# Performance work log

Measured on AMD Instinct MI355X. Metric: run time of the kernel, lower is better.

## Reference

```python
import jax, jax.numpy as jnp
import numpy as np

H = 256      # hidden_dim
D = 64       # dim_dynamic
ND = 2       # num_dynamic
PR = 7       # pooler_resolution
S = PR * PR  # 49 spatial positions
B = 4800     # N * nr_boxes
P = H * D    # num_params
EPS = 1e-5


def setup_inputs() -> dict:
    key = jax.random.key(0)
    ks = jax.random.split(key, 32)
    def w(k, shape):
        return jax.random.normal(k, shape, dtype=jnp.float32) * 0.02
    inp = {
        "pro_features": jax.random.normal(ks[0], (1, B, H), jnp.float32),
        "roi_features": jax.random.normal(ks[1], (S, B, H), jnp.float32),
        "pos_xywh": jax.random.normal(ks[2], (1, B, H), jnp.float32),
        "pos_img": jax.random.normal(ks[3], (S, B, H), jnp.float32),
        "pos_local": jax.random.uniform(ks[4], (PR, PR), jnp.float32),
        "bboxes_xywh": jax.random.uniform(ks[5], (B, 4), jnp.float32, minval=0.2, maxval=1.0),
        # dynamic_layer: H -> ND*P
        "Wd": w(ks[6], (H, ND * P)), "bd": jnp.zeros((ND * P,), jnp.float32),
        # query_scale MLP (2 layers, H->H->H)
        "Wqs1": w(ks[7], (H, H)), "bqs1": jnp.zeros((H,), jnp.float32),
        "Wqs2": w(ks[8], (H, H)), "bqs2": jnp.zeros((H,), jnp.float32),
        # ref_point_head MLP (2 layers, H->H->2)
        "Wr1": w(ks[9], (H, H)), "br1": jnp.zeros((H,), jnp.float32),
        "Wr2": w(ks[10], (H, 2)), "br2": jnp.zeros((2,), jnp.float32),
        # ca_qpos_proj / ca_kpos_proj
        "Wq": w(ks[11], (H, H)), "bq": jnp.zeros((H,), jnp.float32),
        "Wk": w(ks[12], (H, H)), "bk": jnp.zeros((H,), jnp.float32),
        # layer norms
        "g1": jnp.ones((D,), jnp.float32), "be1": jnp.zeros((D,), jnp.float32),
        "g2": jnp.ones((H,), jnp.float32), "be2": jnp.zeros((H,), jnp.float32),
        "g3": jnp.ones((H,), jnp.float32), "be3": jnp.zeros((H,), jnp.float32),
        # out_layer: (H*S) -> H
        "Wo": w(ks[13], (H * S, H)), "bo": jnp.zeros((H,), jnp.float32),
    }
    return inp


def _ln(x, g, b):
    m = jnp.mean(x, axis=-1, keepdims=True)
    v = jnp.mean((x - m) ** 2, axis=-1, keepdims=True)
    return (x - m) * jax.lax.rsqrt(v + EPS) * g + b


def reference(pro_features, roi_features, pos_xywh, pos_img, pos_local, bboxes_xywh,
              Wd, bd, Wqs1, bqs1, Wqs2, bqs2, Wr1, br1, Wr2, br2,
              Wq, bq, Wk, bk, g1, be1, g2, be2, g3, be3, Wo, bo):
    # (S,B,H) -> (B,S,H)
    features_pos = jnp.transpose(pos_img @ Wq + bq, (1, 0, 2))
    features = jnp.transpose(roi_features, (1, 0, 2))
    # dynamic parameters: (1,B,ND*P) -> (B,1,ND*P)
    parameters = jnp.transpose(pro_features @ Wd + bd, (1, 0, 2))
    # query_scale MLP
    pos_t = jax.nn.relu(pro_features @ Wqs1 + bqs1) @ Wqs2 + bqs2  # (1,B,H)
    px = pos_xywh[..., :H] * pos_t                                 # (1,B,H)
    # ref_point_head -> sigmoid
    ref = jax.nn.sigmoid(jax.nn.relu(pro_features @ Wr1 + br1) @ Wr2 + br2)  # (1,B,2)
    bb = bboxes_xywh.reshape(1, -1, 4)
    hi = px[..., H // 2:] * (ref[..., 0] / bb[..., 2])[..., None]
    lo = px[..., :H // 2] * (ref[..., 1] / bb[..., 3])[..., None]
    px = jnp.concatenate([lo, hi], axis=-1)
    # (B,1,H) * (1,S,1) -> (B,S,H)
    px = jnp.transpose(px, (1, 0, 2)) * pos_local.reshape(-1)[None, :, None]
    param1_pos = px @ Wk + bk                                      # (B,S,H)
    param1 = parameters[:, :, :P].reshape(-1, H, D)                # (B,H,D)
    param2 = parameters[:, :, P:].reshape(-1, D, H)                # (B,D,H)
    f = jnp.einsum('bsh,bhd->bsd', features, param1)               # (B,S,D)
    fp = jnp.sum(features_pos * param1_pos, axis=-1)               # (B,S)
    f = f + fp[:, :, None]
    f = jax.nn.relu(_ln(f, g1, be1))
    f = jnp.einsum('bsd,bdh->bsh', f, param2)                      # (B,S,H)
    f = jax.nn.relu(_ln(f, g2, be2))
    f = f.reshape(f.shape[0], -1) @ Wo + bo                        # (B,H)
    f = jax.nn.relu(_ln(f, g3, be3))
    return f
```

## Files before the change

kernel.cpp:

```cpp
#include <hip/hip_runtime.h>
#include <hip/hip_bf16.h>

#define HH 256
#define DD 64
#define SS 49
#define BB 4800
#define PP 16384
#define NDP 32768
#define KWO 12544
#define MPAD 4864
#define SK 8
#define KCH 1568

typedef unsigned int u32;
typedef unsigned short u16;
typedef __attribute__((ext_vector_type(8))) short bf16x8;
typedef __attribute__((ext_vector_type(4))) float f32x4;

__device__ __forceinline__ float bf2f(__hip_bfloat16 h) { return __bfloat162float(h); }

__device__ __forceinline__ void load_lds16(const void* g, void* l) {
  __builtin_amdgcn_global_load_lds(
      (const __attribute__((address_space(1))) unsigned int*)g,
      (__attribute__((address_space(3))) unsigned int*)l, 16, 0, 0);
}

__device__ __forceinline__ int nperm(int n) {
  if (n < PP) { int h = n >> 6, d = n & 63; return d * HH + h; }
  int r = n - PP; int d = r >> 8, h = r & 255; return PP + h * DD + d;
}

__device__ __forceinline__ float wave_sum64(float v) {
#pragma unroll
  for (int off = 32; off > 0; off >>= 1) v += __shfl_xor(v, off);
  return v;
}

__device__ __forceinline__ float block_sum256(float v, float* red) {
  v = wave_sum64(v);
  int w = threadIdx.x >> 6;
  if ((threadIdx.x & 63) == 0) red[w] = v;
  __syncthreads();
  float r = red[0] + red[1] + red[2] + red[3];
  __syncthreads();
  return r;
}

__global__ void k0_prep(const float* __restrict__ Wq, const float* __restrict__ bk,
                        const float* __restrict__ bq, float* __restrict__ w2c2) {
  __shared__ float red[4];
  int k = blockIdx.x, h = threadIdx.x;
  float v = Wq[k * HH + h];
  float s = block_sum256(v * bk[h], red);
  if (h == 0) w2c2[k] = s;
  if (k == 0) {
    float s2 = block_sum256(bq[h] * bk[h], red);
    if (h == 0) w2c2[HH] = s2;
  }
}

__global__ __launch_bounds__(256) void kc_w1(
    const float* __restrict__ Wqs1, const float* __restrict__ Wqs2,
    const float* __restrict__ Wr1, const float* __restrict__ Wk,
    const float* __restrict__ Wq,
    u16* __restrict__ w1t, u16* __restrict__ w2t, u16* __restrict__ wr1t,
    u16* __restrict__ wkt, u16* __restrict__ wqh) {
  int t = threadIdx.x;
  int zi = blockIdx.z;
  if (zi == 4) {
    int row = blockIdx.y * 32 + (t >> 3), col = blockIdx.x * 32 + (t & 7) * 4;
    float4 v = *(const float4*)&Wq[row * HH + col];
    union { u16 u[4]; uint2 q; } pk;
    __hip_bfloat16 hb;
    hb = __float2bfloat16(v.x); pk.u[0] = *(u16*)&hb;
    hb = __float2bfloat16(v.y); pk.u[1] = *(u16*)&hb;
    hb = __float2bfloat16(v.z); pk.u[2] = *(u16*)&hb;
    hb = __float2bfloat16(v.w); pk.u[3] = *(u16*)&hb;
    *(uint2*)&wqh[row * HH + col] = pk.q;
    return;
  }
  const float* src = (zi == 0) ? Wqs1 : (zi == 1) ? Wqs2 : (zi == 2) ? Wr1 : Wk;
  u16* dst = (zi == 0) ? w1t : (zi == 1) ? w2t : (zi == 2) ? wr1t : wkt;
  __shared__ float tile[32][33];
  int n0 = blockIdx.x * 32, k0 = blockIdx.y * 32;
  {
    int kk = t >> 3, nn = (t & 7) * 4;
    float4 v = *(const float4*)&src[(k0 + kk) * HH + n0 + nn];
    tile[kk][nn + 0] = v.x;
    tile[kk][nn + 1] = v.y;
    tile[kk][nn + 2] = v.z;
    tile[kk][nn + 3] = v.w;
  }
  __syncthreads();
  {
    int nn = t >> 3, kk = (t & 7) * 4;
    union { u16 u[4]; uint2 q; } pk;
#pragma unroll
    for (int i = 0; i < 4; ++i) {
      __hip_bfloat16 hb = __float2bfloat16(tile[kk + i][nn]);
      pk.u[i] = *(u16*)&hb;
    }
    *(uint2*)&dst[(n0 + nn) * HH + k0 + kk] = pk.q;
  }
}

__device__ __forceinline__ void g_gemm(const u16* aLb, const u16* __restrict__ Bg,
                                       int wm, int wn, int lg, int lr,
                                       f32x4 acc[2][4]) {
#pragma unroll
  for (int k0 = 0; k0 < HH; k0 += 32) {
    int colb = (k0 + (lg << 3)) << 1;
    bf16x8 af[2];
#pragma unroll
    for (int mi = 0; mi < 2; ++mi) {
      int row = wm * 32 + mi * 16 + lr;
      af[mi] = *(const bf16x8*)((const char*)aLb + (row << 9) +
                                (colb ^ ((row & 7) << 4)));
    }
    bf16x8 bfr[4];
#pragma unroll
    for (int ni = 0; ni < 4; ++ni) {
      int n = wn * 64 + ni * 16 + lr;
      bfr[ni] = *(const bf16x8*)&Bg[n * HH + k0 + (lg << 3)];
    }
#pragma unroll
    for (int mi = 0; mi < 2; ++mi)
#pragma unroll
      for (int ni = 0; ni < 4; ++ni)
        acc[mi][ni] = __builtin_amdgcn_mfma_f32_16x16x32_bf16(af[mi], bfr[ni], acc[mi][ni], 0, 0, 0);
  }
}

__device__ __forceinline__ void c_write(u16* xLb, f32x4 acc[2][4],
                                        const float* __restrict__ bias, bool dorelu,
                                        int wm, int wn, int lg, int lr) {
#pragma unroll
  for (int ni = 0; ni < 4; ++ni) {
    int col = wn * 64 + ni * 16 + lr;
    float bv = bias ? bias[col] : 0.f;
#pragma unroll
    for (int mi = 0; mi < 2; ++mi) {
#pragma unroll
      for (int j = 0; j < 4; ++j) {
        int row = wm * 32 + mi * 16 + (lg << 2) + j;
        float v = acc[mi][ni][j] + bv;
        if (dorelu) v = fmaxf(v, 0.f);
        __hip_bfloat16 hb = __float2bfloat16(v);
        *(u16*)((char*)xLb + (row << 9) + (((col << 1)) ^ ((row & 7) << 4))) = *(u16*)&hb;
      }
    }
  }
}

__global__ __launch_bounds__(512) void k1_mfma(
    const u16* __restrict__ proh, const float* __restrict__ posx,
    const float* __restrict__ bbox,
    const u16* __restrict__ w1t, const u16* __restrict__ w2t,
    const u16* __restrict__ wr1t, const u16* __restrict__ wkt,
    const u16* __restrict__ wqh,
    const float* __restrict__ bqs1, const float* __restrict__ bqs2,
    const float* __restrict__ br1, const float* __restrict__ Wr2,
    const float* __restrict__ br2, const float* __restrict__ bq,
    float* __restrict__ z, float* __restrict__ c1) {
  __shared__ u16 aL[16384];
  __shared__ u16 xL[16384];
  __shared__ float red0[512], red1[512];
  __shared__ float scLoL[64], scHiL[64];
  const int t = threadIdx.x;
  const int w = t >> 6, l = t & 63;
  const int lg = l >> 4, lr = l & 15;
  const int wm = w >> 2, wn = w & 3;
  const int m0 = blockIdx.x * 64;

#pragma unroll
  for (int i = 0; i < 4; ++i) {
    int c = i * 512 + t;
    int a = c * 16;
    int row = a >> 9, x0 = a & 511;
    int src = (m0 + row) * HH + ((x0 ^ ((row & 7) << 4)) >> 1);
    load_lds16(proh + src, (char*)aL + (size_t)(i * 512 + (w << 6)) * 16);
  }
  __syncthreads();

  {
    f32x4 acc[2][4] = {};
    g_gemm(aL, wr1t, wm, wn, lg, lr, acc);
    c_write(xL, acc, br1, true, wm, wn, lg, lr);
  }
  __syncthreads();
  {
    int row = t & 63, seg = t >> 6;
    float s0 = 0.f, s1 = 0.f;
#pragma unroll 8
    for (int hh = 0; hh < 32; ++hh) {
      int h = seg * 32 + hh;
      float rv = bf2f(*(const __hip_bfloat16*)((const char*)xL + (row << 9) +
                                               (((h << 1)) ^ ((row & 7) << 4))));
      s0 = fmaf(rv, Wr2[h * 2 + 0], s0);
      s1 = fmaf(rv, Wr2[h * 2 + 1], s1);
    }
    red0[row * 8 + seg] = s0;
    red1[row * 8 + seg] = s1;
  }
  __syncthreads();
  if (t < 64) {
    float s0 = br2[0], s1 = br2[1];
#pragma unroll
    for (int k = 0; k < 8; ++k) {
      s0 += red0[t * 8 + k];
      s1 += red1[t * 8 + k];
    }
    float r0 = 1.f / (1.f + __expf(-s0));
    float r1 = 1.f / (1.f + __expf(-s1));
    scHiL[t] = r0 / bbox[(m0 + t) * 4 + 2];
    scLoL[t] = r1 / bbox[(m0 + t) * 4 + 3];
  }
  f32x4 acc1[2][4] = {};
  g_gemm(aL, w1t, wm, wn, lg, lr, acc1);
  __syncthreads();
  c_write(xL, acc1, bqs1, true, wm, wn, lg, lr);
  __syncthreads();
  f32x4 accp[2][4] = {};
  g_gemm(xL, w2t, wm, wn, lg, lr, accp);
  __syncthreads();
#pragma unroll
  for (int ni = 0; ni < 4; ++ni) {
    int col = wn * 64 + ni * 16 + lr;
    float bv = bqs2[col];
#pragma unroll
    for (int mi = 0; mi < 2; ++mi) {
#pragma unroll
      for (int j = 0; j < 4; ++j) {
        int row = wm * 32 + mi * 16 + (lg << 2) + j;
        float pt = accp[mi][ni][j] + bv;
        float sc = (col < 128) ? scLoL[row] : scHiL[row];
        float v = posx[(m0 + row) * HH + col] * pt * sc;
        __hip_bfloat16 hb = __float2bfloat16(v);
        *(u16*)((char*)aL + (row << 9) + (((col << 1)) ^ ((row & 7) << 4))) = *(u16*)&hb;
      }
    }
  }
  __syncthreads();
  {
    f32x4 acc[2][4] = {};
    g_gemm(aL, wkt, wm, wn, lg, lr, acc);
    c_write(xL, acc, nullptr, false, wm, wn, lg, lr);
  }
  __syncthreads();
  {
    int row = t & 63, seg = t >> 6;
    float s0 = 0.f;
#pragma unroll 8
    for (int hh = 0; hh < 32; ++hh) {
      int h = seg * 32 + hh;
      float yv = bf2f(*(const __hip_bfloat16*)((const char*)xL + (row << 9) +
                                               (((h << 1)) ^ ((row & 7) << 4))));
      s0 = fmaf(yv, bq[h], s0);
    }
    red0[row * 8 + seg] = s0;
  }
  f32x4 accz[2][4] = {};
  g_gemm(xL, wqh, wm, wn, lg, lr, accz);
  __syncthreads();
  if (t < 64) {
    float s = 0.f;
#pragma unroll
    for (int k = 0; k < 8; ++k) s += red0[t * 8 + k];
    c1[m0 + t] = s;
  }
#pragma unroll
  for (int ni = 0; ni < 4; ++ni) {
    int col = wn * 64 + ni * 16 + lr;
#pragma unroll
    for (int mi = 0; mi < 2; ++mi) {
#pragma unroll
      for (int j = 0; j < 4; ++j) {
        int row = wm * 32 + mi * 16 + (lg << 2) + j;
        z[(size_t)(m0 + row) * HH + col] = accz[mi][ni][j];
      }
    }
  }
}

__global__ __launch_bounds__(256) void k2_fp(
    const float* __restrict__ posi, const float* __restrict__ posl,
    const float* __restrict__ z, const float* __restrict__ c1,
    const float* __restrict__ w2c2, float* __restrict__ fp) {
  int b = blockIdx.x, t = threadIdx.x;
  int l = t & 63, w = t >> 6;
  float4 zv = *(const float4*)&z[b * HH + l * 4];
  float4 wv = *(const float4*)&w2c2[l * 4];
  float c1b = c1[b];
  float c2 = w2c2[HH];
  for (int s = w; s < SS; s += 4) {
    float4 pi = *(const float4*)&posi[((size_t)s * BB + b) * HH + l * 4];
    float d1 = pi.x * zv.x + pi.y * zv.y + pi.z * zv.z + pi.w * zv.w;
    float d2 = pi.x * wv.x + pi.y * wv.y + pi.z * wv.z + pi.w * wv.w;
#pragma unroll
    for (int off = 32; off > 0; off >>= 1) {
      d1 += __shfl_xor(d1, off);
      d2 += __shfl_xor(d2, off);
    }
    if (l == 0) fp[b * SS + s] = posl[s] * (d1 + c1b) + d2 + c2;
  }
}

__global__ __launch_bounds__(256) void kc_pro(const float* __restrict__ pro,
                                              u16* __restrict__ proh) {
  int tg = blockIdx.x * 256 + threadIdx.x;
  int e0 = tg * 8;
  int row = e0 >> 8;
  union { u16 u[8]; uint4 v; } pk;
  if (row < BB) {
    float4 v0 = *(const float4*)&pro[e0];
    float4 v1 = *(const float4*)&pro[e0 + 4];
    float vv[8] = {v0.x, v0.y, v0.z, v0.w, v1.x, v1.y, v1.z, v1.w};
#pragma unroll
    for (int i = 0; i < 8; ++i) {
      __hip_bfloat16 hb = __float2bfloat16(vv[i]);
      pk.u[i] = *(u16*)&hb;
    }
  } else {
    pk.v = make_uint4(0, 0, 0, 0);
  }
  *(uint4*)&proh[e0] = pk.v;
}

__global__ __launch_bounds__(256) void kc_wdt(const float* __restrict__ Wd,
                                              u16* __restrict__ wdt) {
  __shared__ float tile[32][33];
  int n0 = blockIdx.x * 32;
  int k0 = blockIdx.y * 32;
  int t = threadIdx.x;
  {
    int kk = t >> 3, nn = (t & 7) * 4;
    float4 v = *(const float4*)&Wd[(size_t)(k0 + kk) * NDP + n0 + nn];
    tile[kk][nn + 0] = v.x;
    tile[kk][nn + 1] = v.y;
    tile[kk][nn + 2] = v.z;
    tile[kk][nn + 3] = v.w;
  }
  __syncthreads();
  {
    int nn = t >> 3, kk = (t & 7) * 4;
    union { u16 u[4]; uint2 v; } pk;
#pragma unroll
    for (int i = 0; i < 4; ++i) {
      __hip_bfloat16 hb = __float2bfloat16(tile[kk + i][nn]);
      pk.u[i] = *(u16*)&hb;
    }
    int np = nperm(n0 + nn);
    *(uint2*)&wdt[(size_t)np * HH + k0 + kk] = pk.v;
  }
}

__global__ void kc_bdp(const float* __restrict__ bd, float* __restrict__ bdp) {
  int n = blockIdx.x * 256 + threadIdx.x;
  bdp[nperm(n)] = bd[n];
}

__global__ __launch_bounds__(256) void kc_wot(const float* __restrict__ Wo,
                                              u16* __restrict__ wot) {
  __shared__ float tile[32][33];
  int k0 = blockIdx.x * 32;
  int n0 = blockIdx.y * 32;
  int t = threadIdx.x;
  {
    int kk = t >> 3, nn = (t & 7) * 4;
    float4 v = *(const float4*)&Wo[(size_t)(k0 + kk) * HH + n0 + nn];
    tile[kk][nn + 0] = v.x;
    tile[kk][nn + 1] = v.y;
    tile[kk][nn + 2] = v.z;
    tile[kk][nn + 3] = v.w;
  }
  __syncthreads();
  {
    int nn = t >> 3, kk = (t & 7) * 4;
    union { u16 u[4]; uint2 v; } pk;
#pragma unroll
    for (int i = 0; i < 4; ++i) {
      __hip_bfloat16 hb = __float2bfloat16(tile[kk + i][nn]);
      pk.u[i] = *(u16*)&hb;
    }
    *(uint2*)&wot[(size_t)(n0 + nn) * KWO + k0 + kk] = pk.v;
  }
}

__global__ __launch_bounds__(256) void k3_mfma(const u16* __restrict__ proh,
                                               const u16* __restrict__ wdt,
                                               const float* __restrict__ bdp,
                                               u16* __restrict__ params) {
  __shared__ char smem[32768];
  const int t = threadIdx.x;
  const int w = t >> 6, l = t & 63;
  const int n0 = blockIdx.x * 128;
  const int m0 = blockIdx.y * 128;
  const int wr = w >> 1, wc = w & 1;
  f32x4 acc[4][4] = {};

  auto stage = [&](int buf, int k0) {
    u16* Ab = (u16*)(smem + buf * 16384);
    u16* Bb = Ab + 4096;
#pragma unroll
    for (int i = 0; i < 2; ++i) {
      int c = i * 256 + t;
      int r = c >> 2, kq = (c & 3) * 8;
      int wbase = (i * 256 + (w << 6)) * 8;
      load_lds16(proh + (size_t)(m0 + r) * HH + k0 + kq, Ab + wbase);
      load_lds16(wdt + (size_t)(n0 + r) * HH + k0 + kq, Bb + wbase);
    }
  };

  stage(0, 0);
  __syncthreads();
  for (int ks = 0; ks < 8; ++ks) {
    int cur = ks & 1;
    if (ks < 7) stage(cur ^ 1, (ks + 1) * 32);
    const u16* Al = (const u16*)(smem + cur * 16384);
    const u16* Bl = Al + 4096;
    bf16x8 af[4], bfr[4];
#pragma unroll
    for (int mi = 0; mi < 4; ++mi)
      af[mi] = *(const bf16x8*)&Al[(wr * 64 + mi * 16 + (l & 15)) * 32 + (l >> 4) * 8];
#pragma unroll
    for (int ni = 0; ni < 4; ++ni)
      bfr[ni] = *(const bf16x8*)&Bl[(wc * 64 + ni * 16 + (l & 15)) * 32 + (l >> 4) * 8];
#pragma unroll
    for (int mi = 0; mi < 4; ++mi)
#pragma unroll
      for (int ni = 0; ni < 4; ++ni)
        acc[mi][ni] = __builtin_amdgcn_mfma_f32_16x16x32_bf16(af[mi], bfr[ni], acc[mi][ni], 0, 0, 0);
    __syncthreads();
  }
  u16* cb = (u16*)smem;
#pragma unroll
  for (int ni = 0; ni < 4; ++ni) {
    int col = wc * 64 + ni * 16 + (l & 15);
    float bias = bdp[n0 + col];
#pragma unroll
    for (int mi = 0; mi < 4; ++mi) {
#pragma unroll
      for (int j = 0; j < 4; ++j) {
        int row = wr * 64 + mi * 16 + ((l >> 4) << 2) + j;
        __hip_bfloat16 hb = __float2bfloat16(acc[mi][ni][j] + bias);
        cb[row * 128 + col] = *(u16*)&hb;
      }
    }
  }
  __syncthreads();
#pragma unroll
  for (int i = 0; i < 8; ++i) {
    int idx = i * 256 + t;
    int row = idx >> 4, cc = (idx & 15) * 8;
    if (m0 + row < BB)
      *(uint4*)&params[(size_t)(m0 + row) * NDP + n0 + cc] = *(const uint4*)&cb[row * 128 + cc];
  }
}

__global__ __launch_bounds__(256) void k4_mfma(
    const float* __restrict__ roi, const u16* __restrict__ params,
    const float* __restrict__ fpbuf,
    const float* __restrict__ g1, const float* __restrict__ be1,
    const float* __restrict__ g2, const float* __restrict__ be2,
    u16* __restrict__ f2ws) {
  __shared__ u16 bufP[4096];
  __shared__ u16 bufF[4096];
  __shared__ float fpL[64];
  __shared__ float g1L[64], b1L[64], g2L[256], b2L[256];

  const int b = blockIdx.x;
  const int t = threadIdx.x;
  const int w = t >> 6, l = t & 63;
  const int lg = l >> 4, lr = l & 15;
  const u16* p1g = params + (size_t)b * NDP;
  const u16* p2g = params + (size_t)b * NDP + PP;

  f32x4 acc1[4] = {};
#pragma unroll
  for (int q = 0; q < 4; ++q) {
    const int hoff = q * 64;
#pragma unroll
    for (int i = 0; i < 2; ++i) {
      int c = i * 256 + t;
      int row = c >> 3, x0 = (c & 7) * 16;
      load_lds16(p1g + row * HH + hoff + ((x0 ^ ((row & 7) << 4)) >> 1),
                 (char*)bufP + (size_t)(i * 256 + (w << 6)) * 16);
    }
#pragma unroll
    for (int i = 0; i < 4; ++i) {
      int idx = i * 256 + t;
      int row = idx >> 4, c4 = (idx & 15) << 2;
      union { u16 u[4]; unsigned long long v; } pk;
      if (row < SS) {
        float4 v = *(const float4*)&roi[((size_t)row * BB + b) * HH + hoff + c4];
        __hip_bfloat16 h0 = __float2bfloat16(v.x), h1 = __float2bfloat16(v.y);
        __hip_bfloat16 h2 = __float2bfloat16(v.z), h3 = __float2bfloat16(v.w);
        pk.u[0] = *(u16*)&h0; pk.u[1] = *(u16*)&h1;
        pk.u[2] = *(u16*)&h2; pk.u[3] = *(u16*)&h3;
      } else {
        pk.v = 0ull;
      }
      int ab = (row << 7) + (((c4 << 1)) ^ ((row & 7) << 4));
      *(unsigned long long*)((char*)bufF + ab) = pk.v;
    }
    if (q == 0) {
      if (t < 64) {
        fpL[t] = (t < SS) ? fpbuf[b * SS + t] : 0.f;
        g1L[t] = g1[t];
        b1L[t] = be1[t];
      }
      g2L[t] = g2[t];
      b2L[t] = be2[t];
    }
    __syncthreads();
#pragma unroll
    for (int kk = 0; kk < 64; kk += 32) {
      int arow = w * 16 + lr;
      const bf16x8 af = *(const bf16x8*)((const char*)bufF + (arow << 7) +
                                         ((((kk + (lg << 3)) << 1)) ^ ((arow & 7) << 4)));
      bf16x8 bfr[4];
#pragma unroll
      for (int ni = 0; ni < 4; ++ni) {
        int brow = ni * 16 + lr;
        bfr[ni] = *(const bf16x8*)((const char*)bufP + (brow << 7) +
                                   ((((kk + (lg << 3)) << 1)) ^ ((brow & 7) << 4)));
      }
#pragma unroll
      for (int ni = 0; ni < 4; ++ni)
        acc1[ni] = __builtin_amdgcn_mfma_f32_16x16x32_bf16(af, bfr[ni], acc1[ni], 0, 0, 0);
    }
    __syncthreads();
  }

#pragma unroll
  for (int i = 0; i < 2; ++i) {
    int c = i * 256 + t;
    int row = c >> 3, x0 = (c & 7) * 16;
    load_lds16(p2g + row * DD + ((x0 ^ ((row & 7) << 4)) >> 1),
               (char*)bufP + (size_t)(i * 256 + (w << 6)) * 16);
  }

  u16* f1L = bufF;
#pragma unroll
  for (int j = 0; j < 4; ++j) {
    int s = w * 16 + (lg << 2) + j;
    float fpv = fpL[s];
    float x[4], sum = 0.f, sq = 0.f;
#pragma unroll
    for (int ni = 0; ni < 4; ++ni) {
      x[ni] = acc1[ni][j] + fpv;
      sum += x[ni];
      sq += x[ni] * x[ni];
    }
#pragma unroll
    for (int off = 1; off < 16; off <<= 1) {
      sum += __shfl_xor(sum, off);
      sq += __shfl_xor(sq, off);
    }
    float m = sum * (1.f / 64.f);
    float rs = rsqrtf(sq * (1.f / 64.f) - m * m + 1e-5f);
#pragma unroll
    for (int ni = 0; ni < 4; ++ni) {
      int d = ni * 16 + lr;
      float o = fmaxf((x[ni] - m) * rs * g1L[d] + b1L[d], 0.f);
      __hip_bfloat16 hb = __float2bfloat16(o);
      *(u16*)((char*)f1L + (s << 7) + ((d << 1) ^ ((s & 7) << 4))) = *(u16*)&hb;
    }
  }
  __syncthreads();

  f32x4 acc2[16] = {};
#pragma unroll
  for (int nq = 0; nq < 4; ++nq) {
    if (nq > 0) {
      __syncthreads();
#pragma unroll
      for (int i = 0; i < 2; ++i) {
        int c = i * 256 + t;
        int row = c >> 3, x0 = (c & 7) * 16;
        load_lds16(p2g + (nq * 64 + row) * DD + ((x0 ^ ((row & 7) << 4)) >> 1),
                   (char*)bufP + (size_t)(i * 256 + (w << 6)) * 16);
      }
      __syncthreads();
    }
#pragma unroll
    for (int kk = 0; kk < 64; kk += 32) {
      int arow = w * 16 + lr;
      const bf16x8 af = *(const bf16x8*)((const char*)f1L + (arow << 7) +
                                         ((((kk + (lg << 3)) << 1)) ^ ((arow & 7) << 4)));
#pragma unroll
      for (int ni = 0; ni < 4; ++ni) {
        int brow = ni * 16 + lr;
        const bf16x8 bfr = *(const bf16x8*)((const char*)bufP + (brow << 7) +
                                            ((((kk + (lg << 3)) << 1)) ^ ((brow & 7) << 4)));
        acc2[nq * 4 + ni] = __builtin_amdgcn_mfma_f32_16x16x32_bf16(af, bfr, acc2[nq * 4 + ni], 0, 0, 0);
      }
    }
  }

#pragma unroll
  for (int j = 0; j < 4; ++j) {
    int s = w * 16 + (lg << 2) + j;
    float sum = 0.f, sq = 0.f;
#pragma unroll
    for (int ni = 0; ni < 16; ++ni) {
      float v = acc2[ni][j];
      sum += v;
      sq += v * v;
    }
#pragma unroll
    for (int off = 1; off < 16; off <<= 1) {
      sum += __shfl_xor(sum, off);
      sq += __shfl_xor(sq, off);
    }
    float m = sum * (1.f / 256.f);
    float rs = rsqrtf(sq * (1.f / 256.f) - m * m + 1e-5f);
    if (s < SS) {
#pragma unroll
      for (int ni = 0; ni < 16; ++ni) {
        int h = (ni >> 2) * 64 + (ni & 3) * 16 + lr;
        float o = fmaxf((acc2[ni][j] - m) * rs * g2L[h] + b2L[h], 0.f);
        __hip_bfloat16 hb = __float2bfloat16(o);
        f2ws[(size_t)b * KWO + s * HH + h] = *(u16*)&hb;
      }
    }
  }
}

__global__ __launch_bounds__(256) void k5_mfma(const u16* __restrict__ f2,
                                               const u16* __restrict__ wot,
                                               float* __restrict__ part) {
  __shared__ char smem[40960];
  const int t = threadIdx.x;
  const int w = t >> 6, l = t & 63;
  const int lg = l >> 4, lr = l & 15;
  const int sk = blockIdx.x;
  const int m0 = blockIdx.y * 64;
  const size_t kbase = (size_t)sk * KCH;
  const int wr = w >> 1, wc = w & 1;
  f32x4 acc[2][8] = {};

  auto stage = [&](int buf, int k0) {
    u16* Al = (u16*)(smem + buf * 20480);
    u16* Bl = Al + 2048;
    {
      int r = t >> 2, kq = (t & 3) * 8;
      int wbase = (w << 6) * 8;
      load_lds16(f2 + (size_t)(m0 + r) * KWO + kbase + k0 + kq, Al + wbase);
    }
#pragma unroll
    for (int i = 0; i < 4; ++i) {
      int c = i * 256 + t;
      int r = c >> 2, kq = (c & 3) * 8;
      int wbase = (i * 256 + (w << 6)) * 8;
      load_lds16(wot + (size_t)r * KWO + kbase + k0 + kq, Bl + wbase);
    }
  };

  stage(0, 0);
  __syncthreads();
  for (int ks = 0; ks < 49; ++ks) {
    int cur = ks & 1;
    if (ks < 48) stage(cur ^ 1, (ks + 1) * 32);
    const u16* Al = (const u16*)(smem + cur * 20480);
    const u16* Bl = Al + 2048;
    bf16x8 af[2], bfr[8];
#pragma unroll
    for (int mi = 0; mi < 2; ++mi)
      af[mi] = *(const bf16x8*)&Al[(wr * 32 + mi * 16 + lr) * 32 + lg * 8];
#pragma unroll
    for (int ni = 0; ni < 8; ++ni)
      bfr[ni] = *(const bf16x8*)&Bl[(wc * 128 + ni * 16 + lr) * 32 + lg * 8];
#pragma unroll
    for (int mi = 0; mi < 2; ++mi)
#pragma unroll
      for (int ni = 0; ni < 8; ++ni)
        acc[mi][ni] = __builtin_amdgcn_mfma_f32_16x16x32_bf16(af[mi], bfr[ni], acc[mi][ni], 0, 0, 0);
    __syncthreads();
  }
#pragma unroll
  for (int mi = 0; mi < 2; ++mi) {
#pragma unroll
    for (int j = 0; j < 4; ++j) {
      int m = m0 + wr * 32 + mi * 16 + (lg << 2) + j;
#pragma unroll
      for (int ni = 0; ni < 8; ++ni) {
        int n = wc * 128 + ni * 16 + lr;
        part[((size_t)sk * BB + m) * HH + n] = acc[mi][ni][j];
      }
    }
  }
}

__global__ __launch_bounds__(256) void k5r_ln3(
    const float* __restrict__ part, const float* __restrict__ bo,
    const float* __restrict__ g3, const float* __restrict__ be3,
    float* __restrict__ out) {
  __shared__ float red[4];
  int b = blockIdx.x, t = threadIdx.x;
  float v = bo[t];
#pragma unroll
  for (int sk = 0; sk < SK; ++sk) v += part[((size_t)sk * BB + b) * HH + t];
  float m = block_sum256(v, red) * (1.f / HH);
  float d = v - m;
  float var = block_sum256(d * d, red) * (1.f / HH);
  out[b * HH + t] = fmaxf(fmaf(d * rsqrtf(var + 1e-5f), g3[t], be3[t]), 0.f);
}

extern "C" void kernel_launch(void* const* d_in, const int* in_sizes, int n_in,
                              void* d_out, int out_size, void* d_ws, size_t ws_size,
                              hipStream_t stream) {
  const float* pro  = (const float*)d_in[0];
  const float* roi  = (const float*)d_in[1];
  const float* posx = (const float*)d_in[2];
  const float* posi = (const float*)d_in[3];
  const float* posl = (const float*)d_in[4];
  const float* bbox = (const float*)d_in[5];
  const float* Wd   = (const float*)d_in[6];
  const float* bd   = (const float*)d_in[7];
  const float* Wqs1 = (const float*)d_in[8];
  const float* bqs1 = (const float*)d_in[9];
  const float* Wqs2 = (const float*)d_in[10];
  const float* bqs2 = (const float*)d_in[11];
  const float* Wr1  = (const float*)d_in[12];
  const float* br1  = (const float*)d_in[13];
  const float* Wr2  = (const float*)d_in[14];
  const float* br2  = (const float*)d_in[15];
  const float* Wq   = (const float*)d_in[16];
  const float* bq   = (const float*)d_in[17];
  const float* Wk   = (const float*)d_in[18];
  const float* bk   = (const float*)d_in[19];
  const float* g1   = (const float*)d_in[20];
  const float* be1  = (const float*)d_in[21];
  const float* g2   = (const float*)d_in[22];
  const float* be2  = (const float*)d_in[23];
  const float* g3   = (const float*)d_in[24];
  const float* be3  = (const float*)d_in[25];
  const float* Wo   = (const float*)d_in[26];
  const float* bo   = (const float*)d_in[27];

  char* ws = (char*)d_ws;
  u16* w1t  = (u16*)(ws + 0ull);
  u16* w2t  = (u16*)(ws + 131072ull);
  u16* wr1t = (u16*)(ws + 262144ull);
  u16* wkt  = (u16*)(ws + 393216ull);
  u16* wqh  = (u16*)(ws + 524288ull);
  u16* params = (u16*)(ws + 0ull);
  float* part = (float*)(ws + 0ull);
  u16* f2ws   = (u16*)(ws + 314572800ull);
  u16* proh   = (u16*)(ws + 314572800ull);
  u16* wdt    = (u16*)(ws + 317063168ull);
  float* z    = (float*)(ws + 434995200ull);
  u16* wot    = (u16*)(ws + 434995200ull);
  float* bdp  = (float*)(ws + 441417728ull);
  float* fp   = (float*)(ws + 444825600ull);
  float* c1   = (float*)(ws + 445766400ull);
  float* w2c2 = (float*)(ws + 446047744ull);

  kc_pro<<<dim3(MPAD * HH / 8 / 256), dim3(256), 0, stream>>>(pro, proh);
  kc_w1<<<dim3(8, 8, 5), dim3(256), 0, stream>>>(Wqs1, Wqs2, Wr1, Wk, Wq,
                                                 w1t, w2t, wr1t, wkt, wqh);
  k0_prep<<<dim3(256), dim3(256), 0, stream>>>(Wq, bk, bq, w2c2);
  k1_mfma<<<dim3(BB / 64), dim3(512), 0, stream>>>(proh, posx, bbox, w1t, w2t, wr1t,
                                                   wkt, wqh, bqs1, bqs2, br1, Wr2,
                                                   br2, bq, z, c1);
  k2_fp<<<dim3(BB), dim3(256), 0, stream>>>(posi, posl, z, c1, w2c2, fp);
  kc_wot<<<dim3(KWO / 32, HH / 32), dim3(256), 0, stream>>>(Wo, wot);
  kc_wdt<<<dim3(NDP / 32, HH / 32), dim3(256), 0, stream>>>(Wd, wdt);
  kc_bdp<<<dim3(NDP / 256), dim3(256), 0, stream>>>(bd, bdp);
  k3_mfma<<<dim3(NDP / 128, MPAD / 128), dim3(256), 0, stream>>>(proh, wdt, bdp, params);
  k4_mfma<<<dim3(BB), dim3(256), 0, stream>>>(roi, params, fp, g1, be1, g2, be2, f2ws);
  k5_mfma<<<dim3(SK, BB / 64), dim3(256), 0, stream>>>(f2ws, wot, part);
  k5r_ln3<<<dim3(BB), dim3(256), 0, stream>>>(part, bo, g3, be3, (float*)d_out);
}
```

Baseline: 542.6 us.

## Shrink k1 row tile to 16 for more blocks; store split-K partials as bf16

The k1 MLP kernel now handles 16 rows per 256-thread block instead of 64 rows per 512-thread block. This launches 300 blocks instead of 75, so more CUs get work on a chip with many CUs, at the cost of reloading the B weights for each smaller tile. Separately, the split-K partials from the out-layer GEMM are stored as bf16 instead of fp32. That halves the partial-sum write and read traffic in k5 and k5r but adds rounding error before LayerNorm3.

```diff
diff --git a/kernel.cpp b/kernel.cpp
--- a/kernel.cpp
+++ b/kernel.cpp
@@ -18,6 +18,11 @@
 typedef __attribute__((ext_vector_type(4))) float f32x4;
 
 __device__ __forceinline__ float bf2f(__hip_bfloat16 h) { return __bfloat162float(h); }
+
+__device__ __forceinline__ u16 f2bf(float v) {
+  __hip_bfloat16 hb = __float2bfloat16(v);
+  return *(u16*)&hb;
+}
 
 __device__ __forceinline__ void load_lds16(const void* g, void* l) {
   __builtin_amdgcn_global_load_lds(
@@ -71,11 +76,8 @@
     int row = blockIdx.y * 32 + (t >> 3), col = blockIdx.x * 32 + (t & 7) * 4;
     float4 v = *(const float4*)&Wq[row * HH + col];
     union { u16 u[4]; uint2 q; } pk;
-    __hip_bfloat16 hb;
-    hb = __float2bfloat16(v.x); pk.u[0] = *(u16*)&hb;
-    hb = __float2bfloat16(v.y); pk.u[1] = *(u16*)&hb;
-    hb = __float2bfloat16(v.z); pk.u[2] = *(u16*)&hb;
-    hb = __float2bfloat16(v.w); pk.u[3] = *(u16*)&hb;
+    pk.u[0] = f2bf(v.x); pk.u[1] = f2bf(v.y);
+    pk.u[2] = f2bf(v.z); pk.u[3] = f2bf(v.w);
     *(uint2*)&wqh[row * HH + col] = pk.q;
     return;
   }
@@ -96,27 +98,18 @@
     int nn = t >> 3, kk = (t & 7) * 4;
     union { u16 u[4]; uint2 q; } pk;
 #pragma unroll
-    for (int i = 0; i < 4; ++i) {
-      __hip_bfloat16 hb = __float2bfloat16(tile[kk + i][nn]);
-      pk.u[i] = *(u16*)&hb;
-    }
+    for (int i = 0; i < 4; ++i) pk.u[i] = f2bf(tile[kk + i][nn]);
     *(uint2*)&dst[(n0 + nn) * HH + k0 + kk] = pk.q;
   }
 }
 
-__device__ __forceinline__ void g_gemm(const u16* aLb, const u16* __restrict__ Bg,
-                                       int wm, int wn, int lg, int lr,
-                                       f32x4 acc[2][4]) {
+__device__ __forceinline__ void g_gemm16(const u16* aLb, const u16* __restrict__ Bg,
+                                         int wn, int lg, int lr, f32x4 acc[4]) {
 #pragma unroll
   for (int k0 = 0; k0 < HH; k0 += 32) {
     int colb = (k0 + (lg << 3)) << 1;
-    bf16x8 af[2];
-#pragma unroll
-    for (int mi = 0; mi < 2; ++mi) {
-      int row = wm * 32 + mi * 16 + lr;
-      af[mi] = *(const bf16x8*)((const char*)aLb + (row << 9) +
-                                (colb ^ ((row & 7) << 4)));
-    }
+    const bf16x8 af = *(const bf16x8*)((const char*)aLb + (lr << 9) +
+                                       (colb ^ ((lr & 7) << 4)));
     bf16x8 bfr[4];
 #pragma unroll
     for (int ni = 0; ni < 4; ++ni) {
@@ -124,35 +117,29 @@
       bfr[ni] = *(const bf16x8*)&Bg[n * HH + k0 + (lg << 3)];
     }
 #pragma unroll
-    for (int mi = 0; mi < 2; ++mi)
-#pragma unroll
-      for (int ni = 0; ni < 4; ++ni)
-        acc[mi][ni] = __builtin_amdgcn_mfma_f32_16x16x32_bf16(af[mi], bfr[ni], acc[mi][ni], 0, 0, 0);
-  }
-}
-
-__device__ __forceinline__ void c_write(u16* xLb, f32x4 acc[2][4],
-                                        const float* __restrict__ bias, bool dorelu,
-                                        int wm, int wn, int lg, int lr) {
+    for (int ni = 0; ni < 4; ++ni)
+      acc[ni] = __builtin_amdgcn_mfma_f32_16x16x32_bf16(af, bfr[ni], acc[ni], 0, 0, 0);
+  }
+}
+
+__device__ __forceinline__ void c_write16(u16* xLb, f32x4 acc[4],
+                                          const float* __restrict__ bias, bool dorelu,
+                                          int wn, int lg, int lr) {
 #pragma unroll
   for (int ni = 0; ni < 4; ++ni) {
     int col = wn * 64 + ni * 16 + lr;
     float bv = bias ? bias[col] : 0.f;
 #pragma unroll
-    for (int mi = 0; mi < 2; ++mi) {
-#pragma unroll
-      for (int j = 0; j < 4; ++j) {
-        int row = wm * 32 + mi * 16 + (lg << 2) + j;
-        float v = acc[mi][ni][j] + bv;
-        if (dorelu) v = fmaxf(v, 0.f);
-        __hip_bfloat16 hb = __float2bfloat16(v);
-        *(u16*)((char*)xLb + (row << 9) + (((col << 1)) ^ ((row & 7) << 4))) = *(u16*)&hb;
-      }
-    }
-  }
-}
-
-__global__ __launch_bounds__(512) void k1_mfma(
+    for (int j = 0; j < 4; ++j) {
+      int row = (lg << 2) + j;
+      float v = acc[ni][j] + bv;
+      if (dorelu) v = fmaxf(v, 0.f);
+      *(u16*)((char*)xLb + (row << 9) + (((col << 1)) ^ ((row & 7) << 4))) = f2bf(v);
+    }
+  }
+}
+
+__global__ __launch_bounds__(256) void k1_mfma(
     const u16* __restrict__ proh, const float* __restrict__ posx,
     const float* __restrict__ bbox,
     const u16* __restrict__ w1t, const u16* __restrict__ w2t,
@@ -162,122 +149,115 @@
     const float* __restrict__ br1, const float* __restrict__ Wr2,
     const float* __restrict__ br2, const float* __restrict__ bq,
     float* __restrict__ z, float* __restrict__ c1) {
-  __shared__ u16 aL[16384];
-  __shared__ u16 xL[16384];
-  __shared__ float red0[512], red1[512];
-  __shared__ float scLoL[64], scHiL[64];
+  __shared__ u16 aL[4096];
+  __shared__ u16 xL[4096];
+  __shared__ float red0[256], red1[256];
+  __shared__ float scLoL[16], scHiL[16];
   const int t = threadIdx.x;
   const int w = t >> 6, l = t & 63;
   const int lg = l >> 4, lr = l & 15;
-  const int wm = w >> 2, wn = w & 3;
-  const int m0 = blockIdx.x * 64;
-
-#pragma unroll
-  for (int i = 0; i < 4; ++i) {
-    int c = i * 512 + t;
+  const int wn = w;
+  const int m0 = blockIdx.x * 16;
+
+#pragma unroll
+  for (int i = 0; i < 2; ++i) {
+    int c = i * 256 + t;
     int a = c * 16;
     int row = a >> 9, x0 = a & 511;
     int src = (m0 + row) * HH + ((x0 ^ ((row & 7) << 4)) >> 1);
-    load_lds16(proh + src, (char*)aL + (size_t)(i * 512 + (w << 6)) * 16);
-  }
-  __syncthreads();
-
-  {
-    f32x4 acc[2][4] = {};
-    g_gemm(aL, wr1t, wm, wn, lg, lr, acc);
-    c_write(xL, acc, br1, true, wm, wn, lg, lr);
-  }
-  __syncthreads();
-  {
-    int row = t & 63, seg = t >> 6;
+    load_lds16(proh + src, (char*)aL + (size_t)(i * 256 + (w << 6)) * 16);
+  }
+  __syncthreads();
+
+  {
+    f32x4 acc[4] = {};
+    g_gemm16(aL, wr1t, wn, lg, lr, acc);
+    c_write16(xL, acc, br1, true, wn, lg, lr);
+  }
+  __syncthreads();
+  {
+    int row = t & 15, seg = t >> 4;
     float s0 = 0.f, s1 = 0.f;
-#pragma unroll 8
-    for (int hh = 0; hh < 32; ++hh) {
-      int h = seg * 32 + hh;
+#pragma unroll
+    for (int hh = 0; hh < 16; ++hh) {
+      int h = seg * 16 + hh;
       float rv = bf2f(*(const __hip_bfloat16*)((const char*)xL + (row << 9) +
                                                (((h << 1)) ^ ((row & 7) << 4))));
       s0 = fmaf(rv, Wr2[h * 2 + 0], s0);
       s1 = fmaf(rv, Wr2[h * 2 + 1], s1);
     }
-    red0[row * 8 + seg] = s0;
-    red1[row * 8 + seg] = s1;
-  }
-  __syncthreads();
-  if (t < 64) {
+    red0[row * 16 + seg] = s0;
+    red1[row * 16 + seg] = s1;
+  }
+  __syncthreads();
+  if (t < 16) {
     float s0 = br2[0], s1 = br2[1];
 #pragma unroll
-    for (int k = 0; k < 8; ++k) {
-      s0 += red0[t * 8 + k];
-      s1 += red1[t * 8 + k];
+    for (int k = 0; k < 16; ++k) {
+      s0 += red0[t * 16 + k];
+      s1 += red1[t * 16 + k];
     }
     float r0 = 1.f / (1.f + __expf(-s0));
     float r1 = 1.f / (1.f + __expf(-s1));
     scHiL[t] = r0 / bbox[(m0 + t) * 4 + 2];
     scLoL[t] = r1 / bbox[(m0 + t) * 4 + 3];
   }
-  f32x4 acc1[2][4] = {};
-  g_gemm(aL, w1t, wm, wn, lg, lr, acc1);
-  __syncthreads();
-  c_write(xL, acc1, bqs1, true, wm, wn, lg, lr);
-  __syncthreads();
-  f32x4 accp[2][4] = {};
-  g_gemm(xL, w2t, wm, wn, lg, lr, accp);
+  f32x4 acc1[4] = {};
+  g_gemm16(aL, w1t, wn, lg, lr, acc1);
+  __syncthreads();
+  c_write16(xL, acc1, bqs1, true, wn, lg, lr);
+  __syncthreads();
+  f32x4 accp[4] = {};
+  g_gemm16(xL, w2t, wn, lg, lr, accp);
   __syncthreads();
 #pragma unroll
   for (int ni = 0; ni < 4; ++ni) {
     int col = wn * 64 + ni * 16 + lr;
     float bv = bqs2[col];
 #pragma unroll
-    for (int mi = 0; mi < 2; ++mi) {
-#pragma unroll
-      for (int j = 0; j < 4; ++j) {
-        int row = wm * 32 + mi * 16 + (lg << 2) + j;
-        float pt = accp[mi][ni][j] + bv;
-        float sc = (col < 128) ? scLoL[row] : scHiL[row];
-        float v = posx[(m0 + row) * HH + col] * pt * sc;
-        __hip_bfloat16 hb = __float2bfloat16(v);
-        *(u16*)((char*)aL + (row << 9) + (((col << 1)) ^ ((row & 7) << 4))) = *(u16*)&hb;
-      }
-    }
-  }
-  __syncthreads();
-  {
-    f32x4 acc[2][4] = {};
-    g_gemm(aL, wkt, wm, wn, lg, lr, acc);
-    c_write(xL, acc, nullptr, false, wm, wn, lg, lr);
-  }
-  __syncthreads();
-  {
-    int row = t & 63, seg = t >> 6;
+    for (int j = 0; j < 4; ++j) {
+      int row = (lg << 2) + j;
+      float pt = accp[ni][j] + bv;
+      float sc = (col < 128) ? scLoL[row] : scHiL[row];
+      float v = posx[(m0 + row) * HH + col] * pt * sc;
+      *(u16*)((char*)aL + (row << 9) + (((col << 1)) ^ ((row & 7) << 4))) = f2bf(v);
+    }
+  }
+  __syncthreads();
+  {
+    f32x4 acc[4] = {};
+    g_gemm16(aL, wkt, wn, lg, lr, acc);
+    c_write16(xL, acc, nullptr, false, wn, lg, lr);
+  }
+  __syncthreads();
+  {
+    int row = t & 15, seg = t >> 4;
     float s0 = 0.f;
-#pragma unroll 8
-    for (int hh = 0; hh < 32; ++hh) {
-      int h = seg * 32 + hh;
+#pragma unroll
+    for (int hh = 0; hh < 16; ++hh) {
+      int h = seg * 16 + hh;
       float yv = bf2f(*(const __hip_bfloat16*)((const char*)xL + (row << 9) +
                                                (((h << 1)) ^ ((row & 7) << 4))));
       s0 = fmaf(yv, bq[h], s0);
     }
-    red0[row * 8 + seg] = s0;
-  }
-  f32x4 accz[2][4] = {};
-  g_gemm(xL, wqh, wm, wn, lg, lr, accz);
-  __syncthreads();
-  if (t < 64) {
+    red0[row * 16 + seg] = s0;
+  }
+  f32x4 accz[4] = {};
+  g_gemm16(xL, wqh, wn, lg, lr, accz);
+  __syncthreads();
+  if (t < 16) {
     float s = 0.f;
 #pragma unroll
-    for (int k = 0; k < 8; ++k) s += red0[t * 8 + k];
+    for (int k = 0; k < 16; ++k) s += red0[t * 16 + k];
     c1[m0 + t] = s;
   }
 #pragma unroll
   for (int ni = 0; ni < 4; ++ni) {
     int col = wn * 64 + ni * 16 + lr;
 #pragma unroll
-    for (int mi = 0; mi < 2; ++mi) {
-#pragma unroll
-      for (int j = 0; j < 4; ++j) {
-        int row = wm * 32 + mi * 16 + (lg << 2) + j;
-        z[(size_t)(m0 + row) * HH + col] = accz[mi][ni][j];
-      }
+    for (int j = 0; j < 4; ++j) {
+      int row = (lg << 2) + j;
+      z[(size_t)(m0 + row) * HH + col] = accz[ni][j];
     }
   }
 }
@@ -316,10 +296,7 @@
     float4 v1 = *(const float4*)&pro[e0 + 4];
     float vv[8] = {v0.x, v0.y, v0.z, v0.w, v1.x, v1.y, v1.z, v1.w};
 #pragma unroll
-    for (int i = 0; i < 8; ++i) {
-      __hip_bfloat16 hb = __float2bfloat16(vv[i]);
-      pk.u[i] = *(u16*)&hb;
-    }
+    for (int i = 0; i < 8; ++i) pk.u[i] = f2bf(vv[i]);
   } else {
     pk.v = make_uint4(0, 0, 0, 0);
   }
@@ -345,10 +322,7 @@
     int nn = t >> 3, kk = (t & 7) * 4;
     union { u16 u[4]; uint2 v; } pk;
 #pragma unroll
-    for (int i = 0; i < 4; ++i) {
-      __hip_bfloat16 hb = __float2bfloat16(tile[kk + i][nn]);
-      pk.u[i] = *(u16*)&hb;
-    }
+    for (int i = 0; i < 4; ++i) pk.u[i] = f2bf(tile[kk + i][nn]);
     int np = nperm(n0 + nn);
     *(uint2*)&wdt[(size_t)np * HH + k0 + kk] = pk.v;
   }
@@ -378,10 +352,7 @@
     int nn = t >> 3, kk = (t & 7) * 4;
     union { u16 u[4]; uint2 v; } pk;
 #pragma unroll
-    for (int i = 0; i < 4; ++i) {
-      __hip_bfloat16 hb = __float2bfloat16(tile[kk + i][nn]);
-      pk.u[i] = *(u16*)&hb;
-    }
+    for (int i = 0; i < 4; ++i) pk.u[i] = f2bf(tile[kk + i][nn]);
     *(uint2*)&wot[(size_t)(n0 + nn) * KWO + k0 + kk] = pk.v;
   }
 }
@@ -442,8 +413,7 @@
 #pragma unroll
       for (int j = 0; j < 4; ++j) {
         int row = wr * 64 + mi * 16 + ((l >> 4) << 2) + j;
-        __hip_bfloat16 hb = __float2bfloat16(acc[mi][ni][j] + bias);
-        cb[row * 128 + col] = *(u16*)&hb;
+        cb[row * 128 + col] = f2bf(acc[mi][ni][j] + bias);
       }
     }
   }
@@ -493,10 +463,8 @@
       union { u16 u[4]; unsigned long long v; } pk;
       if (row < SS) {
         float4 v = *(const float4*)&roi[((size_t)row * BB + b) * HH + hoff + c4];
-        __hip_bfloat16 h0 = __float2bfloat16(v.x), h1 = __float2bfloat16(v.y);
-        __hip_bfloat16 h2 = __float2bfloat16(v.z), h3 = __float2bfloat16(v.w);
-        pk.u[0] = *(u16*)&h0; pk.u[1] = *(u16*)&h1;
-        pk.u[2] = *(u16*)&h2; pk.u[3] = *(u16*)&h3;
+        pk.u[0] = f2bf(v.x); pk.u[1] = f2bf(v.y);
+        pk.u[2] = f2bf(v.z); pk.u[3] = f2bf(v.w);
       } else {
         pk.v = 0ull;
       }
@@ -563,8 +531,7 @@
     for (int ni = 0; ni < 4; ++ni) {
       int d = ni * 16 + lr;
       float o = fmaxf((x[ni] - m) * rs * g1L[d] + b1L[d], 0.f);
-      __hip_bfloat16 hb = __float2bfloat16(o);
-      *(u16*)((char*)f1L + (s << 7) + ((d << 1) ^ ((s & 7) << 4))) = *(u16*)&hb;
+      *(u16*)((char*)f1L + (s << 7) + ((d << 1) ^ ((s & 7) << 4))) = f2bf(o);
     }
   }
   __syncthreads();
@@ -620,8 +587,7 @@
       for (int ni = 0; ni < 16; ++ni) {
         int h = (ni >> 2) * 64 + (ni & 3) * 16 + lr;
         float o = fmaxf((acc2[ni][j] - m) * rs * g2L[h] + b2L[h], 0.f);
-        __hip_bfloat16 hb = __float2bfloat16(o);
-        f2ws[(size_t)b * KWO + s * HH + h] = *(u16*)&hb;
+        f2ws[(size_t)b * KWO + s * HH + h] = f2bf(o);
       }
     }
   }
@@ -629,7 +595,7 @@
 
 __global__ __launch_bounds__(256) void k5_mfma(const u16* __restrict__ f2,
                                                const u16* __restrict__ wot,
-                                               float* __restrict__ part) {
+                                               u16* __restrict__ part) {
   __shared__ char smem[40960];
   const int t = threadIdx.x;
   const int w = t >> 6, l = t & 63;
@@ -686,21 +652,22 @@
 #pragma unroll
       for (int ni = 0; ni < 8; ++ni) {
         int n = wc * 128 + ni * 16 + lr;
-        part[((size_t)sk * BB + m) * HH + n] = acc[mi][ni][j];
+        part[((size_t)sk * BB + m) * HH + n] = f2bf(acc[mi][ni][j]);
       }
     }
   }
 }
 
 __global__ __launch_bounds__(256) void k5r_ln3(
-    const float* __restrict__ part, const float* __restrict__ bo,
+    const u16* __restrict__ part, const float* __restrict__ bo,
     const float* __restrict__ g3, const float* __restrict__ be3,
     float* __restrict__ out) {
   __shared__ float red[4];
   int b = blockIdx.x, t = threadIdx.x;
   float v = bo[t];
 #pragma unroll
-  for (int sk = 0; sk < SK; ++sk) v += part[((size_t)sk * BB + b) * HH + t];
+  for (int sk = 0; sk < SK; ++sk)
+    v += bf2f(*(const __hip_bfloat16*)&part[((size_t)sk * BB + b) * HH + t]);
   float m = block_sum256(v, red) * (1.f / HH);
   float d = v - m;
   float var = block_sum256(d * d, red) * (1.f / HH);
@@ -746,7 +713,7 @@
   u16* wkt  = (u16*)(ws + 393216ull);
   u16* wqh  = (u16*)(ws + 524288ull);
   u16* params = (u16*)(ws + 0ull);
-  float* part = (float*)(ws + 0ull);
+  u16* part   = (u16*)(ws + 0ull);
   u16* f2ws   = (u16*)(ws + 314572800ull);
   u16* proh   = (u16*)(ws + 314572800ull);
   u16* wdt    = (u16*)(ws + 317063168ull);
@@ -761,7 +728,7 @@
   kc_w1<<<dim3(8, 8, 5), dim3(256), 0, stream>>>(Wqs1, Wqs2, Wr1, Wk, Wq,
                                                  w1t, w2t, wr1t, wkt, wqh);
   k0_prep<<<dim3(256), dim3(256), 0, stream>>>(Wq, bk, bq, w2c2);
-  k1_mfma<<<dim3(BB / 64), dim3(512), 0, stream>>>(proh, posx, bbox, w1t, w2t, wr1t,
+  k1_mfma<<<dim3(BB / 16), dim3(256), 0, stream>>>(proh, posx, bbox, w1t, w2t, wr1t,
                                                    wkt, wqh, bqs1, bqs2, br1, Wr2,
                                                    br2, bq, z, c1);
   k2_fp<<<dim3(BB), dim3(256), 0, stream>>>(posi, posl, z, c1, w2c2, fp);
```

After: 531.2 us. 1.02x faster.
